# Performance work log

Hardware: AMD Instinct MI355X
Metric: run time of the kernel (lower is better)

## Reference

```python
import jax, jax.numpy as jnp
import numpy as np

D_MODEL = 16
D_STATE = 16
D_CONV = 4
EXPAND = 2
D_INNER = EXPAND * D_MODEL  # 32
DT_RANK = 1                 # ceil(d_model / 16)
H_MLP = 2 * D_MODEL         # MLP hidden = input_dim * 2
EPS = 1e-6
B, L = 16, 8192


def setup_inputs() -> dict:
    key = jax.random.key(0)
    ks = jax.random.split(key, 20)
    g = lambda i, shape, s: jax.random.normal(ks[i], shape, jnp.float32) * s
    # S4D-real init for A_log, as in mamba_ssm
    A_log = jnp.log(jnp.broadcast_to(jnp.arange(1, D_STATE + 1, dtype=jnp.float32), (D_INNER, D_STATE)))
    return {
        "x": jax.random.normal(ks[0], (B, L, D_MODEL), jnp.float32),
        "rms1_w": jnp.ones((D_MODEL,), jnp.float32),
        "in_proj_w": g(1, (D_MODEL, 2 * D_INNER), 0.25),
        "conv_w": g(2, (D_INNER, D_CONV), 0.3),
        "conv_b": g(3, (D_INNER,), 0.05),
        "x_proj_w": g(4, (D_INNER, DT_RANK + 2 * D_STATE), 0.2),
        "dt_proj_w": g(5, (DT_RANK, D_INNER), 0.5),
        "dt_proj_b": g(6, (D_INNER,), 0.1),
        "A_log": A_log,
        "D_skip": jnp.ones((D_INNER,), jnp.float32),
        "out_proj_w": g(7, (D_INNER, D_MODEL), 0.2),
        "rms2_w": jnp.ones((D_MODEL,), jnp.float32),
        "fc1_w": g(8, (D_MODEL, H_MLP), 0.25),
        "fc1_b": g(9, (H_MLP,), 0.05),
        "fc2_w": g(10, (H_MLP, H_MLP), 0.2),
        "fc2_b": g(11, (H_MLP,), 0.05),
        "fc3_w": g(12, (H_MLP, D_MODEL), 0.2),
        "fc3_b": g(13, (D_MODEL,), 0.05),
    }


def _rmsnorm(h, w):
    v = jnp.mean(h.astype(jnp.float32) ** 2, axis=-1, keepdims=True)
    return w * (h * jax.lax.rsqrt(v + EPS))


def _mamba(x0, in_proj_w, conv_w, conv_b, x_proj_w, dt_proj_w, dt_proj_b, A_log, D_skip, out_proj_w):
    b, l, _ = x0.shape
    xz = x0 @ in_proj_w                      # [B,L,2*Di]
    xm, z = jnp.split(xz, 2, axis=-1)        # each [B,L,Di]
    # causal depthwise conv1d (kernel D_CONV), padding d_conv-1, truncated to L
    xp = jnp.pad(xm, ((0, 0), (D_CONV - 1, 0), (0, 0)))
    xc = conv_b + sum(conv_w[:, k] * xp[:, k:k + l, :] for k in range(D_CONV))
    xc = jax.nn.silu(xc)
    # input-dependent dt, B, C
    proj = xc @ x_proj_w                     # [B,L,dt_rank+2*Ds]
    dt, Bm, Cm = jnp.split(proj, [DT_RANK, DT_RANK + D_STATE], axis=-1)
    dt = jax.nn.softplus(dt @ dt_proj_w + dt_proj_b)   # [B,L,Di]
    A = -jnp.exp(A_log)                      # [Di,Ds]
    deltaA = jnp.exp(dt[..., None] * A)                             # [B,L,Di,Ds]
    deltaBx = dt[..., None] * Bm[:, :, None, :] * xc[..., None]     # [B,L,Di,Ds]
    # sequential selective scan over time (time-major for lax.scan)
    def step(h, inputs):
        dA, dBx, C = inputs                  # [B,Di,Ds],[B,Di,Ds],[B,Ds]
        h = dA * h + dBx
        y = jnp.einsum('bds,bs->bd', h, C)
        return h, y
    h0 = jnp.zeros((b, D_INNER, D_STATE), xc.dtype)
    xs = (deltaA.transpose(1, 0, 2, 3), deltaBx.transpose(1, 0, 2, 3), Cm.transpose(1, 0, 2))
    _, ys = jax.lax.scan(step, h0, xs)       # [L,B,Di]
    y = ys.transpose(1, 0, 2) + D_skip * xc  # [B,L,Di]
    y = y * jax.nn.silu(z)
    return y @ out_proj_w                    # [B,L,Dm]


def reference(x, rms1_w, in_proj_w, conv_w, conv_b, x_proj_w, dt_proj_w, dt_proj_b,
              A_log, D_skip, out_proj_w, rms2_w, fc1_w, fc1_b, fc2_w, fc2_b, fc3_w, fc3_b):
    x0 = _rmsnorm(x, rms1_w)
    x1 = _mamba(x0, in_proj_w, conv_w, conv_b, x_proj_w, dt_proj_w, dt_proj_b, A_log, D_skip, out_proj_w)
    x = x1 + x
    x2 = _rmsnorm(x, rms2_w)
    h = jax.nn.relu(x2 @ fc1_w + fc1_b)
    h = jax.nn.relu(h @ fc2_w + fc2_b)
    x3 = h @ fc3_w + fc3_b
    return x + x3
```

## Files before the change

### kernel.cpp

```cpp
#include <hip/hip_runtime.h>

#define LSEQ 8192
#define NBAT 16
#define DMOD 16
#define DINN 32
#define DSTA 16
#define CL   32
#define NCH  (LSEQ / CL)
#define NCHT (NBAT * NCH)
#define NROWS (NBAT * LSEQ)
#define SUMN ((size_t)NCHT * 512)
#define NSEG 8
#define SEGC (NCH / NSEG)
#define RECU 800
#define LOG2E 1.44269504f

typedef __attribute__((ext_vector_type(8))) short bf16x8;
typedef __attribute__((ext_vector_type(4))) float f32x4;

__device__ __forceinline__ float fsilu(float v) { return v / (1.f + __expf(-v)); }
__device__ __forceinline__ float fsoftplus(float v) {
  return v > 20.f ? v : __logf(1.f + __expf(v));
}
__device__ __forceinline__ unsigned packbf(float a, float b) {
  unsigned r;
  asm("v_cvt_pk_bf16_f32 %0, %1, %2" : "=v"(r) : "v"(a), "v"(b));
  return r;
}
__device__ __forceinline__ short f2bf(float f) {
  return (short)(packbf(f, f) & 0xffffu);
}
__device__ __forceinline__ float bf2f(short s) {
  union { unsigned u; float f; } v;
  v.u = ((unsigned)(unsigned short)s) << 16;
  return v.f;
}
__device__ __forceinline__ float bflo(unsigned u) {
  union { unsigned a; float f; } v; v.a = u << 16; return v.f;
}
__device__ __forceinline__ float bfhi(unsigned u) {
  union { unsigned a; float f; } v; v.a = u & 0xffff0000u; return v.f;
}

__device__ __forceinline__ void load_x_row(const float* __restrict__ x, long r,
                                           float* __restrict__ xr) {
  const float4* xp = reinterpret_cast<const float4*>(x + r * DMOD);
  float4 v0 = xp[0], v1 = xp[1], v2 = xp[2], v3 = xp[3];
  xr[0] = v0.x; xr[1] = v0.y; xr[2] = v0.z; xr[3] = v0.w;
  xr[4] = v1.x; xr[5] = v1.y; xr[6] = v1.z; xr[7] = v1.w;
  xr[8] = v2.x; xr[9] = v2.y; xr[10] = v2.z; xr[11] = v2.w;
  xr[12] = v3.x; xr[13] = v3.y; xr[14] = v3.z; xr[15] = v3.w;
}

__device__ __forceinline__ f32x4 mm(bf16x8 a, bf16x8 b, f32x4 c) {
  return __builtin_amdgcn_mfma_f32_16x16x32_bf16(a, b, c, 0, 0, 0);
}
__device__ __forceinline__ bf16x8 bfrag(const float* __restrict__ W, int ldw,
                                        int coloff, int col, int kg, int kreal) {
  bf16x8 b = {0, 0, 0, 0, 0, 0, 0, 0};
#pragma unroll
  for (int e = 0; e < 8; e++) {
    int k = kg * 8 + e;
    if (k < kreal) b[e] = f2bf(W[k * ldw + coloff + col]);
  }
  return b;
}

__global__ __launch_bounds__(256) void k_prep(
    const float* __restrict__ x, const float* __restrict__ rms1w,
    const float* __restrict__ ipw, const float* __restrict__ cw,
    const float* __restrict__ cb, const float* __restrict__ xpw,
    const float* __restrict__ dtw, const float* __restrict__ dtb,
    const float* __restrict__ A_log, const float* __restrict__ Dskip,
    unsigned* __restrict__ rec, float* __restrict__ Pb,
    float* __restrict__ Hb) {
  __shared__ short xmv[67][36];
  __shared__ short x0b[64][40];
  __shared__ short xcb[64][40];
  int t = threadIdx.x;
  int lane = t & 63, wid = t >> 6;
  int col = lane & 15, kg = lane >> 4;
  long row0 = (long)blockIdx.x * 64;
  int l0 = (int)(row0 & (LSEQ - 1));
  const f32x4 zero4 = {0.f, 0.f, 0.f, 0.f};

  bf16x8 Bip0 = bfrag(ipw, 64, 0, col, kg, 16);
  bf16x8 Bip1 = bfrag(ipw, 64, 16, col, kg, 16);
  bf16x8 Bdt, Bb, Bc;
#pragma unroll
  for (int e = 0; e < 8; e++) {
    int k = kg * 8 + e;
    Bdt[e] = (col == 0) ? f2bf(xpw[k * 33]) : (short)0;
    Bb[e] = f2bf(xpw[k * 33 + 1 + col]);
    Bc[e] = f2bf(xpw[k * 33 + 17 + col]);
  }

  if (t < 128) {
    int row = t >> 1, hf = t & 1;
    const float4* xp =
        reinterpret_cast<const float4*>(x + (row0 + row) * DMOD + hf * 8);
    float4 v0 = xp[0], v1 = xp[1];
    float xr[8] = {v0.x, v0.y, v0.z, v0.w, v1.x, v1.y, v1.z, v1.w};
    float ss = 0.f;
#pragma unroll
    for (int i = 0; i < 8; i++) ss += xr[i] * xr[i];
    ss += __shfl_xor(ss, 1);
    float inv1 = rsqrtf(ss * (1.f / 16.f) + 1e-6f);
    unsigned u[4];
#pragma unroll
    for (int i = 0; i < 4; i++)
      u[i] = packbf(xr[2 * i] * inv1 * rms1w[hf * 8 + 2 * i],
                    xr[2 * i + 1] * inv1 * rms1w[hf * 8 + 2 * i + 1]);
    *reinterpret_cast<uint4*>(&x0b[row][hf * 8]) =
        make_uint4(u[0], u[1], u[2], u[3]);
  } else if (t < 224) {
    int h = (t - 128) >> 5, k = (t - 128) & 31;
    short v = 0;
    if (l0 != 0) {
      float xr[16];
      load_x_row(x, row0 - 3 + h, xr);
      float ss = 0.f;
#pragma unroll
      for (int i = 0; i < 16; i++) ss += xr[i] * xr[i];
      float inv1 = rsqrtf(ss * (1.f / 16.f) + 1e-6f);
      float acc = 0.f;
#pragma unroll
      for (int i = 0; i < 16; i++)
        acc = fmaf(xr[i] * inv1 * rms1w[i], ipw[i * 64 + k], acc);
      v = f2bf(acc);
    }
    xmv[h][k] = v;
  }
  __syncthreads();

  {
    int arow = wid * 16 + col;
    bf16x8 a = {0, 0, 0, 0, 0, 0, 0, 0};
    if (kg < 2) a = *reinterpret_cast<const bf16x8*>(&x0b[arow][kg * 8]);
    f32x4 m0 = mm(a, Bip0, zero4);
    f32x4 m1 = mm(a, Bip1, zero4);
    int orow = 3 + wid * 16 + kg * 4;
#pragma unroll
    for (int reg = 0; reg < 4; reg++) {
      unsigned p = packbf(m0[reg], m1[reg]);
      xmv[orow + reg][col] = (short)(p & 0xffffu);
      xmv[orow + reg][col + 16] = (short)(p >> 16);
    }
  }
  __syncthreads();

  {
    int row = t >> 2, q = t & 3;
    unsigned u[4];
#pragma unroll
    for (int dp = 0; dp < 4; dp++) {
      int d = q * 8 + dp * 2;
      float ce = cb[d], co = cb[d + 1];
#pragma unroll
      for (int k = 0; k < 4; k++) {
        unsigned xu = *reinterpret_cast<const unsigned*>(&xmv[row + k][d]);
        ce = fmaf(cw[d * 4 + k], bflo(xu), ce);
        co = fmaf(cw[(d + 1) * 4 + k], bfhi(xu), co);
      }
      u[dp] = packbf(fsilu(ce), fsilu(co));
    }
    *reinterpret_cast<uint4*>(&xcb[row][q * 8]) =
        make_uint4(u[0], u[1], u[2], u[3]);
  }
  __syncthreads();

  {
    int arow = wid * 16 + col;
    bf16x8 a2 = *reinterpret_cast<const bf16x8*>(&xcb[arow][kg * 8]);
    f32x4 pd = mm(a2, Bdt, zero4);
    f32x4 pb = mm(a2, Bb, zero4);
    f32x4 pc = mm(a2, Bc, zero4);
    int orow = wid * 16 + kg * 4;
#pragma unroll
    for (int reg = 0; reg < 4; reg++) {
      unsigned p = packbf(pb[reg], pc[reg]);
      xmv[orow + reg][col] = (short)(p & 0xffffu);
      xmv[orow + reg][16 + col] = (short)(p >> 16);
      if (col == 0) xmv[orow + reg][32] = f2bf(pd[reg]);
    }
  }
  __syncthreads();

  {
    int row = t >> 2, q = t & 3;
    float p0 = bf2f(xmv[row][32]);
    unsigned u[4];
#pragma unroll
    for (int dp = 0; dp < 4; dp++) {
      int d = q * 8 + dp * 2;
      u[dp] = packbf(fsoftplus(fmaf(p0, dtw[d], dtb[d])),
                     fsoftplus(fmaf(p0, dtw[d + 1], dtb[d + 1])));
    }
    *reinterpret_cast<uint4*>(&x0b[row][q * 8]) =
        make_uint4(u[0], u[1], u[2], u[3]);
  }
  __syncthreads();

  {
    int ch = t >> 7, b128 = t & 127;
    int d = b128 >> 2, s4 = (b128 & 3) << 2;
    float Ad0 = -__expf(A_log[d * 16 + s4 + 0]) * LOG2E;
    float Ad1 = -__expf(A_log[d * 16 + s4 + 1]) * LOG2E;
    float Ad2 = -__expf(A_log[d * 16 + s4 + 2]) * LOG2E;
    float Ad3 = -__expf(A_log[d * 16 + s4 + 3]) * LOG2E;
    float dskd = Dskip[d];
    bool w0 = (t & 3) == 0;
    float H0 = 0.f, H1 = 0.f, H2 = 0.f, H3 = 0.f, cum = 0.f;
#pragma unroll 4
    for (int li = 0; li < CL; li++) {
      int row = ch * CL + li;
      float dt = bf2f(x0b[row][d]);
      float xcv = bf2f(xcb[row][d]);
      float dx = dt * xcv;
      cum += dt;
      uint2 bu = *reinterpret_cast<const uint2*>(&xmv[row][s4]);
      uint2 cu = *reinterpret_cast<const uint2*>(&xmv[row][16 + s4]);
      float a;
      a = __builtin_amdgcn_exp2f(dt * Ad0); H0 = fmaf(a, H0, dx * bflo(bu.x));
      a = __builtin_amdgcn_exp2f(dt * Ad1); H1 = fmaf(a, H1, dx * bfhi(bu.x));
      a = __builtin_amdgcn_exp2f(dt * Ad2); H2 = fmaf(a, H2, dx * bflo(bu.y));
      a = __builtin_amdgcn_exp2f(dt * Ad3); H3 = fmaf(a, H3, dx * bfhi(bu.y));
      float py = bflo(cu.x) * H0;
      py = fmaf(bfhi(cu.x), H1, py);
      py = fmaf(bflo(cu.y), H2, py);
      py = fmaf(bfhi(cu.y), H3, py);
      py += __shfl_xor(py, 1);
      py += __shfl_xor(py, 2);
      if (w0) xcb[row][d] = f2bf(fmaf(dskd, xcv, py));
    }
    size_t sb_ = (size_t)(blockIdx.x * 2 + ch) * 512 + (size_t)(d * 16 + s4);
    *reinterpret_cast<float4*>(Pb + sb_) = make_float4(
        __builtin_amdgcn_exp2f(cum * Ad0), __builtin_amdgcn_exp2f(cum * Ad1),
        __builtin_amdgcn_exp2f(cum * Ad2), __builtin_amdgcn_exp2f(cum * Ad3));
    *reinterpret_cast<float4*>(Hb + sb_) = make_float4(H0, H1, H2, H3);
  }
  __syncthreads();

  {
    unsigned* rb0 = rec + (size_t)(blockIdx.x * 2) * RECU;
#pragma unroll
    for (int i = 0; i < 7; i++) {
      int idx = i * 256 + t;
      if (idx < 1600) {
        int ch = idx / 800;
        int rem = idx - ch * 800;
        int c = rem >> 5, l = rem & 31;
        int row = ch * 32 + l;
        unsigned val;
        if (c < 16)
          val = *reinterpret_cast<const unsigned*>(&xcb[row][2 * c]);
        else if (c < 24)
          val = *reinterpret_cast<const unsigned*>(&xmv[row][16 + 2 * (c - 16)]);
        else
          val = (unsigned)(unsigned short)xmv[row][32];
        rb0[ch * RECU + rem] = val;
      }
    }
  }
}

__global__ __launch_bounds__(256) void k_seg(float* __restrict__ Pb,
                                             float* __restrict__ Hb,
                                             float* __restrict__ segP,
                                             float* __restrict__ segH) {
  int g = blockIdx.x * 256 + threadIdx.x;
  int b = g >> 12;
  int rem = g & 4095;
  int seg = rem >> 9, st = rem & 511;
  size_t o = ((size_t)(b * NCH + seg * SEGC)) * 512 + st;
  float h = 0.f, p = 1.f;
#pragma unroll 4
  for (int c = 0; c < SEGC; c++) {
    float P = Pb[o], H = Hb[o];
    Pb[o] = p;
    Hb[o] = h;
    h = fmaf(P, h, H);
    p *= P;
    o += 512;
  }
  size_t so = (size_t)(b * NSEG + seg) * 512 + st;
  segP[so] = p;
  segH[so] = h;
}

__global__ __launch_bounds__(256) void k_carry(const float* __restrict__ segP,
                                               const float* __restrict__ segH,
                                               float* __restrict__ carry) {
  int g = blockIdx.x * 256 + threadIdx.x;
  int b = g >> 9, st = g & 511;
  float h = 0.f;
#pragma unroll
  for (int s = 0; s < NSEG; s++) {
    size_t so = (size_t)(b * NSEG + s) * 512 + st;
    carry[so] = h;
    h = fmaf(segP[so], h, segH[so]);
  }
}

__global__ __launch_bounds__(256) void k_mlp(
    const unsigned* __restrict__ rec, const float* __restrict__ x,
    const float* __restrict__ A_log, const float* __restrict__ Pb,
    const float* __restrict__ Hb, const float* __restrict__ carry,
    const float* __restrict__ dtw, const float* __restrict__ dtb,
    const float* __restrict__ rms1w, const float* __restrict__ ipw,
    const float* __restrict__ opw, const float* __restrict__ rms2w,
    const float* __restrict__ f1w, const float* __restrict__ f1b,
    const float* __restrict__ f2w, const float* __restrict__ f2b,
    const float* __restrict__ f3w, const float* __restrict__ f3b,
    float* __restrict__ out) {
  __shared__ float h0L[4 * 516];
  __shared__ float Ads[512];
  __shared__ short sbx[128][24];
  __shared__ short sby[128][40];
  int t = threadIdx.x, bc = blockIdx.x;
  long row0 = (long)bc * 128;

  Ads[t] = -__expf(A_log[t]) * LOG2E;
  Ads[256 + t] = -__expf(A_log[256 + t]) * LOG2E;
#pragma unroll
  for (int i = 0; i < 8; i++) {
    int idx = i * 256 + t;
    int chl = idx >> 9, st = idx & 511;
    int gc = bc * 4 + chl;
    size_t o = (size_t)gc * 512 + st;
    int b = gc >> 8, seg = (gc >> 5) & 7;
    h0L[chl * 516 + st] =
        fmaf(Pb[o], carry[(size_t)(b * NSEG + seg) * 512 + st], Hb[o]);
  }
  {
    int row = t >> 1, hf = t & 1;
    const float4* xp =
        reinterpret_cast<const float4*>(x + (row0 + row) * DMOD + hf * 8);
    float4 v0 = xp[0], v1 = xp[1];
    float xr[8] = {v0.x, v0.y, v0.z, v0.w, v1.x, v1.y, v1.z, v1.w};
    float ss = 0.f;
#pragma unroll
    for (int i = 0; i < 8; i++) ss += xr[i] * xr[i];
    ss += __shfl_xor(ss, 1);
    float inv1 = rsqrtf(ss * (1.f / 16.f) + 1e-6f);
    unsigned u[4];
#pragma unroll
    for (int i = 0; i < 4; i++)
      u[i] = packbf(xr[2 * i] * inv1 * rms1w[hf * 8 + 2 * i],
                    xr[2 * i + 1] * inv1 * rms1w[hf * 8 + 2 * i + 1]);
    *reinterpret_cast<uint4*>(&sbx[t >> 1][hf * 8]) =
        make_uint4(u[0], u[1], u[2], u[3]);
  }
  __syncthreads();

  {
    int ch = t >> 6, half = (t >> 5) & 1, l = t & 31;
    const unsigned* rb = rec + (size_t)(bc * 4 + ch) * RECU;
    float Cv[16];
#pragma unroll
    for (int c = 0; c < 8; c++) {
      unsigned u = rb[(16 + c) * 32 + l];
      Cv[2 * c] = bflo(u);
      Cv[2 * c + 1] = bfhi(u);
    }
    float p0 = bflo(rb[24 * 32 + l]);
    const float* h0c = &h0L[ch * 516];
    int row = ch * 32 + l;
#pragma unroll
    for (int cc = 0; cc < 8; cc++) {
      int c = half * 8 + cc;
      int d0 = 2 * c, d1 = 2 * c + 1;
      float cd0 = fsoftplus(fmaf(p0, dtw[d0], dtb[d0]));
      float cd1 = fsoftplus(fmaf(p0, dtw[d1], dtb[d1]));
#pragma unroll
      for (int dl = 1; dl < 32; dl <<= 1) {
        float u0 = __shfl_up(cd0, dl, 32);
        float u1 = __shfl_up(cd1, dl, 32);
        if (l >= dl) { cd0 += u0; cd1 += u1; }
      }
      unsigned yu = rb[c * 32 + l];
      float acc0 = bflo(yu), acc1 = bfhi(yu);
      int dof0 = d0 * 16, dof1 = d1 * 16;
#pragma unroll
      for (int s = 0; s < 16; s++) {
        float e0 = __builtin_amdgcn_exp2f(Ads[dof0 + s] * cd0);
        float e1 = __builtin_amdgcn_exp2f(Ads[dof1 + s] * cd1);
        acc0 = fmaf(e0 * Cv[s], h0c[dof0 + s], acc0);
        acc1 = fmaf(e1 * Cv[s], h0c[dof1 + s], acc1);
      }
      *reinterpret_cast<unsigned*>(&sby[row][2 * c]) = packbf(acc0, acc1);
    }
  }
  __syncthreads();

  {
    int lane = t & 63, w = t >> 6;
    int col = lane & 15, kg = lane >> 4;
    bf16x8 Bz0 = bfrag(ipw + 32, 64, 0, col, kg, 16);
    bf16x8 Bz1 = bfrag(ipw + 32, 64, 16, col, kg, 16);
    bf16x8 Bop = bfrag(opw, 16, 0, col, kg, 32);
    bf16x8 Bf1_0 = bfrag(f1w, 32, 0, col, kg, 16);
    bf16x8 Bf1_1 = bfrag(f1w, 32, 16, col, kg, 16);
    bf16x8 Bf2_0 = bfrag(f2w, 32, 0, col, kg, 32);
    bf16x8 Bf2_1 = bfrag(f2w, 32, 16, col, kg, 32);
    bf16x8 Bf3 = bfrag(f3w, 16, 0, col, kg, 32);
    float b1_0 = f1b[col], b1_1 = f1b[16 + col];
    float b2_0 = f2b[col], b2_1 = f2b[16 + col];
    float b3c = f3b[col], rw2 = rms2w[col];
    const f32x4 zero4 = {0.f, 0.f, 0.f, 0.f};
#pragma unroll 1
    for (int rt = 0; rt < 2; rt++) {
      int tile0 = w * 32 + rt * 16;
      bf16x8 ax0 = {0, 0, 0, 0, 0, 0, 0, 0};
      if (kg < 2) ax0 = *reinterpret_cast<const bf16x8*>(&sbx[tile0 + col][kg * 8]);
      f32x4 zf0 = mm(ax0, Bz0, zero4);
      f32x4 zf1 = mm(ax0, Bz1, zero4);
#pragma unroll
      for (int reg = 0; reg < 4; reg++) {
        int lrow = tile0 + kg * 4 + reg;
        float y0 = bf2f(sby[lrow][col]);
        float y1 = bf2f(sby[lrow][16 + col]);
        unsigned p = packbf(y0 * fsilu(zf0[reg]), y1 * fsilu(zf1[reg]));
        sby[lrow][col] = (short)(p & 0xffffu);
        sby[lrow][16 + col] = (short)(p >> 16);
      }
      bf16x8 ayo = *reinterpret_cast<const bf16x8*>(&sby[tile0 + col][kg * 8]);
      f32x4 x1f = mm(ayo, Bop, zero4);
      float xres[4];
#pragma unroll
      for (int reg = 0; reg < 4; reg++) {
        long grow = row0 + tile0 + kg * 4 + reg;
        xres[reg] = x1f[reg] + x[grow * 16 + col];
      }
#pragma unroll
      for (int reg = 0; reg < 4; reg++) {
        float ss = xres[reg] * xres[reg];
        ss += __shfl_xor(ss, 1);
        ss += __shfl_xor(ss, 2);
        ss += __shfl_xor(ss, 4);
        ss += __shfl_xor(ss, 8);
        float inv2 = rsqrtf(ss * (1.f / 16.f) + 1e-6f);
        sby[tile0 + kg * 4 + reg][col] = f2bf(xres[reg] * inv2 * rw2);
      }
      bf16x8 ax2 = {0, 0, 0, 0, 0, 0, 0, 0};
      if (kg < 2) ax2 = *reinterpret_cast<const bf16x8*>(&sby[tile0 + col][kg * 8]);
      f32x4 h1f0 = mm(ax2, Bf1_0, zero4);
      f32x4 h1f1 = mm(ax2, Bf1_1, zero4);
#pragma unroll
      for (int reg = 0; reg < 4; reg++) {
        int lrow = tile0 + kg * 4 + reg;
        unsigned p = packbf(fmaxf(h1f0[reg] + b1_0, 0.f),
                            fmaxf(h1f1[reg] + b1_1, 0.f));
        sby[lrow][col] = (short)(p & 0xffffu);
        sby[lrow][16 + col] = (short)(p >> 16);
      }
      bf16x8 ah1 = *reinterpret_cast<const bf16x8*>(&sby[tile0 + col][kg * 8]);
      f32x4 h2f0 = mm(ah1, Bf2_0, zero4);
      f32x4 h2f1 = mm(ah1, Bf2_1, zero4);
#pragma unroll
      for (int reg = 0; reg < 4; reg++) {
        int lrow = tile0 + kg * 4 + reg;
        unsigned p = packbf(fmaxf(h2f0[reg] + b2_0, 0.f),
                            fmaxf(h2f1[reg] + b2_1, 0.f));
        sby[lrow][col] = (short)(p & 0xffffu);
        sby[lrow][16 + col] = (short)(p >> 16);
      }
      bf16x8 ah2 = *reinterpret_cast<const bf16x8*>(&sby[tile0 + col][kg * 8]);
      f32x4 x3f = mm(ah2, Bf3, zero4);
#pragma unroll
      for (int reg = 0; reg < 4; reg++) {
        long grow = row0 + tile0 + kg * 4 + reg;
        out[grow * 16 + col] = xres[reg] + x3f[reg] + b3c;
      }
    }
  }
}

extern "C" void kernel_launch(void* const* d_in, const int* in_sizes, int n_in,
                              void* d_out, int out_size, void* d_ws,
                              size_t ws_size, hipStream_t stream) {
  const float* x = (const float*)d_in[0];
  const float* rms1w = (const float*)d_in[1];
  const float* ipw = (const float*)d_in[2];
  const float* cw = (const float*)d_in[3];
  const float* cb = (const float*)d_in[4];
  const float* xpw = (const float*)d_in[5];
  const float* dtw = (const float*)d_in[6];
  const float* dtb = (const float*)d_in[7];
  const float* A_log = (const float*)d_in[8];
  const float* Dskip = (const float*)d_in[9];
  const float* opw = (const float*)d_in[10];
  const float* rms2w = (const float*)d_in[11];
  const float* f1w = (const float*)d_in[12];
  const float* f1b = (const float*)d_in[13];
  const float* f2w = (const float*)d_in[14];
  const float* f2b = (const float*)d_in[15];
  const float* f3w = (const float*)d_in[16];
  const float* f3b = (const float*)d_in[17];
  float* out = (float*)d_out;

  unsigned* rec = (unsigned*)d_ws;
  float* Pb = (float*)(rec + (size_t)NCHT * RECU);
  float* Hb = Pb + SUMN;
  float* segP = Hb + SUMN;
  float* segH = segP + NBAT * NSEG * 512;
  float* carry = segH + NBAT * NSEG * 512;

  hipLaunchKernelGGL(k_prep, dim3(NROWS / 64), dim3(256), 0, stream, x, rms1w,
                     ipw, cw, cb, xpw, dtw, dtb, A_log, Dskip, rec, Pb, Hb);
  hipLaunchKernelGGL(k_seg, dim3(256), dim3(256), 0, stream, Pb, Hb, segP,
                     segH);
  hipLaunchKernelGGL(k_carry, dim3(32), dim3(256), 0, stream, segP, segH,
                     carry);
  hipLaunchKernelGGL(k_mlp, dim3(NROWS / 128), dim3(256), 0, stream, rec, x,
                     A_log, Pb, Hb, carry, dtw, dtb, rms1w, ipw, opw, rms2w,
                     f1w, f1b, f2w, f2b, f3w, f3b, out);
}
```

Measured before the change: 84.67 us.

## Use one 128-thread block per 32-row chunk in prep and MLP kernels

```diff
diff --git a/kernel.cpp b/kernel.cpp
--- a/kernel.cpp
+++ b/kernel.cpp
@@ -14,6 +14,7 @@
 #define SEGC (NCH / NSEG)
 #define RECU 800
 #define LOG2E 1.44269504f
+#define FENCE() asm volatile("" ::: "memory")
 
 typedef __attribute__((ext_vector_type(8))) short bf16x8;
 typedef __attribute__((ext_vector_type(4))) float f32x4;
@@ -66,7 +67,7 @@
   return b;
 }
 
-__global__ __launch_bounds__(256) void k_prep(
+__global__ __launch_bounds__(128) void k_prep(
     const float* __restrict__ x, const float* __restrict__ rms1w,
     const float* __restrict__ ipw, const float* __restrict__ cw,
     const float* __restrict__ cb, const float* __restrict__ xpw,
@@ -74,14 +75,15 @@
     const float* __restrict__ A_log, const float* __restrict__ Dskip,
     unsigned* __restrict__ rec, float* __restrict__ Pb,
     float* __restrict__ Hb) {
-  __shared__ short xmv[67][36];
-  __shared__ short x0b[64][40];
-  __shared__ short xcb[64][40];
+  __shared__ short XM[35][36];
+  __shared__ short X0[32][32];
+  __shared__ short XC[32][40];
   int t = threadIdx.x;
-  int lane = t & 63, wid = t >> 6;
-  int col = lane & 15, kg = lane >> 4;
-  long row0 = (long)blockIdx.x * 64;
-  int l0 = (int)(row0 & (LSEQ - 1));
+  int l = t & 63, wid = t >> 6;
+  int col = l & 15, kg = l >> 4;
+  int chunk = blockIdx.x;
+  long row0 = (long)chunk * CL;
+  bool first = (chunk & (NCH - 1)) == 0;
   const f32x4 zero4 = {0.f, 0.f, 0.f, 0.f};
 
   bf16x8 Bip0 = bfrag(ipw, 64, 0, col, kg, 16);
@@ -95,56 +97,49 @@
     Bc[e] = f2bf(xpw[k * 33 + 17 + col]);
   }
 
-  if (t < 128) {
-    int row = t >> 1, hf = t & 1;
+  {
+    int row = t >> 2, q = t & 3;
     const float4* xp =
-        reinterpret_cast<const float4*>(x + (row0 + row) * DMOD + hf * 8);
-    float4 v0 = xp[0], v1 = xp[1];
-    float xr[8] = {v0.x, v0.y, v0.z, v0.w, v1.x, v1.y, v1.z, v1.w};
-    float ss = 0.f;
-#pragma unroll
-    for (int i = 0; i < 8; i++) ss += xr[i] * xr[i];
+        reinterpret_cast<const float4*>(x + (row0 + row) * DMOD + q * 4);
+    float4 v = xp[0];
+    float ss = v.x * v.x + v.y * v.y + v.z * v.z + v.w * v.w;
     ss += __shfl_xor(ss, 1);
+    ss += __shfl_xor(ss, 2);
     float inv1 = rsqrtf(ss * (1.f / 16.f) + 1e-6f);
-    unsigned u[4];
-#pragma unroll
-    for (int i = 0; i < 4; i++)
-      u[i] = packbf(xr[2 * i] * inv1 * rms1w[hf * 8 + 2 * i],
-                    xr[2 * i + 1] * inv1 * rms1w[hf * 8 + 2 * i + 1]);
-    *reinterpret_cast<uint4*>(&x0b[row][hf * 8]) =
-        make_uint4(u[0], u[1], u[2], u[3]);
-  } else if (t < 224) {
-    int h = (t - 128) >> 5, k = (t - 128) & 31;
-    short v = 0;
-    if (l0 != 0) {
+    unsigned u0 = packbf(v.x * inv1 * rms1w[q * 4], v.y * inv1 * rms1w[q * 4 + 1]);
+    unsigned u1 = packbf(v.z * inv1 * rms1w[q * 4 + 2], v.w * inv1 * rms1w[q * 4 + 3]);
+    *reinterpret_cast<uint2*>(&X0[row][q * 4]) = make_uint2(u0, u1);
+  }
+  if (t < 96) {
+    int h = t >> 5, k = t & 31;
+    float a0 = 0.f;
+    if (!first) {
       float xr[16];
       load_x_row(x, row0 - 3 + h, xr);
       float ss = 0.f;
 #pragma unroll
       for (int i = 0; i < 16; i++) ss += xr[i] * xr[i];
       float inv1 = rsqrtf(ss * (1.f / 16.f) + 1e-6f);
-      float acc = 0.f;
 #pragma unroll
       for (int i = 0; i < 16; i++)
-        acc = fmaf(xr[i] * inv1 * rms1w[i], ipw[i * 64 + k], acc);
-      v = f2bf(acc);
-    }
-    xmv[h][k] = v;
-  }
-  __syncthreads();
+        a0 = fmaf(xr[i] * inv1 * rms1w[i], ipw[i * 64 + k], a0);
+    }
+    XM[h][k] = f2bf(a0);
+  }
+  FENCE();
 
   {
     int arow = wid * 16 + col;
     bf16x8 a = {0, 0, 0, 0, 0, 0, 0, 0};
-    if (kg < 2) a = *reinterpret_cast<const bf16x8*>(&x0b[arow][kg * 8]);
+    if (kg < 2) a = *reinterpret_cast<const bf16x8*>(&X0[arow][kg * 8]);
     f32x4 m0 = mm(a, Bip0, zero4);
     f32x4 m1 = mm(a, Bip1, zero4);
     int orow = 3 + wid * 16 + kg * 4;
 #pragma unroll
     for (int reg = 0; reg < 4; reg++) {
       unsigned p = packbf(m0[reg], m1[reg]);
-      xmv[orow + reg][col] = (short)(p & 0xffffu);
-      xmv[orow + reg][col + 16] = (short)(p >> 16);
+      XM[orow + reg][col] = (short)(p & 0xffffu);
+      XM[orow + reg][col + 16] = (short)(p >> 16);
     }
   }
   __syncthreads();
@@ -158,37 +153,36 @@
       float ce = cb[d], co = cb[d + 1];
 #pragma unroll
       for (int k = 0; k < 4; k++) {
-        unsigned xu = *reinterpret_cast<const unsigned*>(&xmv[row + k][d]);
+        unsigned xu = *reinterpret_cast<const unsigned*>(&XM[row + k][d]);
         ce = fmaf(cw[d * 4 + k], bflo(xu), ce);
         co = fmaf(cw[(d + 1) * 4 + k], bfhi(xu), co);
       }
       u[dp] = packbf(fsilu(ce), fsilu(co));
     }
-    *reinterpret_cast<uint4*>(&xcb[row][q * 8]) =
-        make_uint4(u[0], u[1], u[2], u[3]);
+    *reinterpret_cast<uint4*>(&XC[row][q * 8]) = make_uint4(u[0], u[1], u[2], u[3]);
   }
   __syncthreads();
 
   {
     int arow = wid * 16 + col;
-    bf16x8 a2 = *reinterpret_cast<const bf16x8*>(&xcb[arow][kg * 8]);
+    bf16x8 a2 = *reinterpret_cast<const bf16x8*>(&XC[arow][kg * 8]);
     f32x4 pd = mm(a2, Bdt, zero4);
     f32x4 pb = mm(a2, Bb, zero4);
     f32x4 pc = mm(a2, Bc, zero4);
-    int orow = wid * 16 + kg * 4;
+    int orow = 3 + wid * 16 + kg * 4;
 #pragma unroll
     for (int reg = 0; reg < 4; reg++) {
       unsigned p = packbf(pb[reg], pc[reg]);
-      xmv[orow + reg][col] = (short)(p & 0xffffu);
-      xmv[orow + reg][16 + col] = (short)(p >> 16);
-      if (col == 0) xmv[orow + reg][32] = f2bf(pd[reg]);
-    }
-  }
-  __syncthreads();
+      XM[orow + reg][col] = (short)(p & 0xffffu);
+      XM[orow + reg][16 + col] = (short)(p >> 16);
+      if (col == 0) XM[orow + reg][32] = f2bf(pd[reg]);
+    }
+  }
+  FENCE();
 
   {
     int row = t >> 2, q = t & 3;
-    float p0 = bf2f(xmv[row][32]);
+    float p0 = bf2f(XM[3 + row][32]);
     unsigned u[4];
 #pragma unroll
     for (int dp = 0; dp < 4; dp++) {
@@ -196,44 +190,40 @@
       u[dp] = packbf(fsoftplus(fmaf(p0, dtw[d], dtb[d])),
                      fsoftplus(fmaf(p0, dtw[d + 1], dtb[d + 1])));
     }
-    *reinterpret_cast<uint4*>(&x0b[row][q * 8]) =
-        make_uint4(u[0], u[1], u[2], u[3]);
+    *reinterpret_cast<uint4*>(&X0[row][q * 8]) = make_uint4(u[0], u[1], u[2], u[3]);
   }
   __syncthreads();
 
   {
-    int ch = t >> 7, b128 = t & 127;
-    int d = b128 >> 2, s4 = (b128 & 3) << 2;
-    float Ad0 = -__expf(A_log[d * 16 + s4 + 0]) * LOG2E;
-    float Ad1 = -__expf(A_log[d * 16 + s4 + 1]) * LOG2E;
-    float Ad2 = -__expf(A_log[d * 16 + s4 + 2]) * LOG2E;
-    float Ad3 = -__expf(A_log[d * 16 + s4 + 3]) * LOG2E;
+    int d = t >> 2, s4 = (t & 3) << 2;
+    float4 al = *reinterpret_cast<const float4*>(A_log + d * DSTA + s4);
+    float Ad0 = -__expf(al.x) * LOG2E, Ad1 = -__expf(al.y) * LOG2E;
+    float Ad2 = -__expf(al.z) * LOG2E, Ad3 = -__expf(al.w) * LOG2E;
     float dskd = Dskip[d];
-    bool w0 = (t & 3) == 0;
+    bool wy = (t & 3) == 0;
     float H0 = 0.f, H1 = 0.f, H2 = 0.f, H3 = 0.f, cum = 0.f;
 #pragma unroll 4
     for (int li = 0; li < CL; li++) {
-      int row = ch * CL + li;
-      float dt = bf2f(x0b[row][d]);
-      float xcv = bf2f(xcb[row][d]);
+      float dt = bf2f(X0[li][d]);
+      float xcv = bf2f(XC[li][d]);
       float dx = dt * xcv;
       cum += dt;
-      uint2 bu = *reinterpret_cast<const uint2*>(&xmv[row][s4]);
-      uint2 cu = *reinterpret_cast<const uint2*>(&xmv[row][16 + s4]);
+      uint2 bu = *reinterpret_cast<const uint2*>(&XM[3 + li][s4]);
+      uint2 cu = *reinterpret_cast<const uint2*>(&XM[3 + li][16 + s4]);
       float a;
       a = __builtin_amdgcn_exp2f(dt * Ad0); H0 = fmaf(a, H0, dx * bflo(bu.x));
       a = __builtin_amdgcn_exp2f(dt * Ad1); H1 = fmaf(a, H1, dx * bfhi(bu.x));
       a = __builtin_amdgcn_exp2f(dt * Ad2); H2 = fmaf(a, H2, dx * bflo(bu.y));
       a = __builtin_amdgcn_exp2f(dt * Ad3); H3 = fmaf(a, H3, dx * bfhi(bu.y));
-      float py = bflo(cu.x) * H0;
-      py = fmaf(bfhi(cu.x), H1, py);
-      py = fmaf(bflo(cu.y), H2, py);
-      py = fmaf(bfhi(cu.y), H3, py);
-      py += __shfl_xor(py, 1);
-      py += __shfl_xor(py, 2);
-      if (w0) xcb[row][d] = f2bf(fmaf(dskd, xcv, py));
-    }
-    size_t sb_ = (size_t)(blockIdx.x * 2 + ch) * 512 + (size_t)(d * 16 + s4);
+      float y = bflo(cu.x) * H0;
+      y = fmaf(bfhi(cu.x), H1, y);
+      y = fmaf(bflo(cu.y), H2, y);
+      y = fmaf(bfhi(cu.y), H3, y);
+      y += __shfl_xor(y, 1);
+      y += __shfl_xor(y, 2);
+      if (wy) XC[li][d] = f2bf(fmaf(dskd, xcv, y));
+    }
+    size_t sb_ = (size_t)chunk * 512 + (size_t)(d * 16 + s4);
     *reinterpret_cast<float4*>(Pb + sb_) = make_float4(
         __builtin_amdgcn_exp2f(cum * Ad0), __builtin_amdgcn_exp2f(cum * Ad1),
         __builtin_amdgcn_exp2f(cum * Ad2), __builtin_amdgcn_exp2f(cum * Ad3));
@@ -242,23 +232,20 @@
   __syncthreads();
 
   {
-    unsigned* rb0 = rec + (size_t)(blockIdx.x * 2) * RECU;
+    unsigned* rb = rec + (size_t)chunk * RECU;
 #pragma unroll
     for (int i = 0; i < 7; i++) {
-      int idx = i * 256 + t;
-      if (idx < 1600) {
-        int ch = idx / 800;
-        int rem = idx - ch * 800;
-        int c = rem >> 5, l = rem & 31;
-        int row = ch * 32 + l;
+      int idx = i * 128 + t;
+      if (idx < 800) {
+        int c = idx >> 5, r = idx & 31;
         unsigned val;
         if (c < 16)
-          val = *reinterpret_cast<const unsigned*>(&xcb[row][2 * c]);
+          val = *reinterpret_cast<const unsigned*>(&XC[r][2 * c]);
         else if (c < 24)
-          val = *reinterpret_cast<const unsigned*>(&xmv[row][16 + 2 * (c - 16)]);
+          val = *reinterpret_cast<const unsigned*>(&XM[3 + r][16 + 2 * (c - 16)]);
         else
-          val = (unsigned)(unsigned short)xmv[row][32];
-        rb0[ch * RECU + rem] = val;
+          val = (unsigned)(unsigned short)XM[3 + r][32];
+        rb[idx] = val;
       }
     }
   }
@@ -302,7 +289,7 @@
   }
 }
 
-__global__ __launch_bounds__(256) void k_mlp(
+__global__ __launch_bounds__(128) void k_mlp(
     const unsigned* __restrict__ rec, const float* __restrict__ x,
     const float* __restrict__ A_log, const float* __restrict__ Pb,
     const float* __restrict__ Hb, const float* __restrict__ carry,
@@ -313,62 +300,60 @@
     const float* __restrict__ f2w, const float* __restrict__ f2b,
     const float* __restrict__ f3w, const float* __restrict__ f3b,
     float* __restrict__ out) {
-  __shared__ float h0L[4 * 516];
   __shared__ float Ads[512];
-  __shared__ short sbx[128][24];
-  __shared__ short sby[128][40];
-  int t = threadIdx.x, bc = blockIdx.x;
-  long row0 = (long)bc * 128;
-
-  Ads[t] = -__expf(A_log[t]) * LOG2E;
-  Ads[256 + t] = -__expf(A_log[256 + t]) * LOG2E;
-#pragma unroll
-  for (int i = 0; i < 8; i++) {
-    int idx = i * 256 + t;
-    int chl = idx >> 9, st = idx & 511;
-    int gc = bc * 4 + chl;
-    size_t o = (size_t)gc * 512 + st;
+  __shared__ float h0w[512];
+  __shared__ short sbx[32][24];
+  __shared__ short sby[32][40];
+  int t = threadIdx.x;
+  int l = t & 63, wid = t >> 6;
+  int gc = blockIdx.x;
+  long row0 = (long)gc * CL;
+
+#pragma unroll
+  for (int i = 0; i < 4; i++) {
+    int idx = i * 128 + t;
+    Ads[idx] = -__expf(A_log[idx]) * LOG2E;
+  }
+  {
+    size_t o = (size_t)gc * 512 + (size_t)(t * 4);
     int b = gc >> 8, seg = (gc >> 5) & 7;
-    h0L[chl * 516 + st] =
-        fmaf(Pb[o], carry[(size_t)(b * NSEG + seg) * 512 + st], Hb[o]);
-  }
-  {
-    int row = t >> 1, hf = t & 1;
+    size_t co = (size_t)(b * NSEG + seg) * 512 + (size_t)(t * 4);
+    float4 pv = *reinterpret_cast<const float4*>(Pb + o);
+    float4 hv = *reinterpret_cast<const float4*>(Hb + o);
+    float4 cv = *reinterpret_cast<const float4*>(carry + co);
+    *reinterpret_cast<float4*>(&h0w[t * 4]) =
+        make_float4(fmaf(pv.x, cv.x, hv.x), fmaf(pv.y, cv.y, hv.y),
+                    fmaf(pv.z, cv.z, hv.z), fmaf(pv.w, cv.w, hv.w));
+  }
+  {
+    int row = t >> 2, q = t & 3;
     const float4* xp =
-        reinterpret_cast<const float4*>(x + (row0 + row) * DMOD + hf * 8);
-    float4 v0 = xp[0], v1 = xp[1];
-    float xr[8] = {v0.x, v0.y, v0.z, v0.w, v1.x, v1.y, v1.z, v1.w};
-    float ss = 0.f;
-#pragma unroll
-    for (int i = 0; i < 8; i++) ss += xr[i] * xr[i];
+        reinterpret_cast<const float4*>(x + (row0 + row) * DMOD + q * 4);
+    float4 v = xp[0];
+    float ss = v.x * v.x + v.y * v.y + v.z * v.z + v.w * v.w;
     ss += __shfl_xor(ss, 1);
+    ss += __shfl_xor(ss, 2);
     float inv1 = rsqrtf(ss * (1.f / 16.f) + 1e-6f);
-    unsigned u[4];
-#pragma unroll
-    for (int i = 0; i < 4; i++)
-      u[i] = packbf(xr[2 * i] * inv1 * rms1w[hf * 8 + 2 * i],
-                    xr[2 * i + 1] * inv1 * rms1w[hf * 8 + 2 * i + 1]);
-    *reinterpret_cast<uint4*>(&sbx[t >> 1][hf * 8]) =
-        make_uint4(u[0], u[1], u[2], u[3]);
+    unsigned u0 = packbf(v.x * inv1 * rms1w[q * 4], v.y * inv1 * rms1w[q * 4 + 1]);
+    unsigned u1 = packbf(v.z * inv1 * rms1w[q * 4 + 2], v.w * inv1 * rms1w[q * 4 + 3]);
+    *reinterpret_cast<uint2*>(&sbx[row][q * 4]) = make_uint2(u0, u1);
   }
   __syncthreads();
 
   {
-    int ch = t >> 6, half = (t >> 5) & 1, l = t & 31;
-    const unsigned* rb = rec + (size_t)(bc * 4 + ch) * RECU;
+    int half = t >> 5, r = t & 31;
+    const unsigned* rb = rec + (size_t)gc * RECU;
     float Cv[16];
 #pragma unroll
     for (int c = 0; c < 8; c++) {
-      unsigned u = rb[(16 + c) * 32 + l];
+      unsigned u = rb[(16 + c) * 32 + r];
       Cv[2 * c] = bflo(u);
       Cv[2 * c + 1] = bfhi(u);
     }
-    float p0 = bflo(rb[24 * 32 + l]);
-    const float* h0c = &h0L[ch * 516];
-    int row = ch * 32 + l;
-#pragma unroll
-    for (int cc = 0; cc < 8; cc++) {
-      int c = half * 8 + cc;
+    float p0 = bflo(rb[24 * 32 + r]);
+#pragma unroll
+    for (int cc = 0; cc < 4; cc++) {
+      int c = half * 4 + cc;
       int d0 = 2 * c, d1 = 2 * c + 1;
       float cd0 = fsoftplus(fmaf(p0, dtw[d0], dtb[d0]));
       float cd1 = fsoftplus(fmaf(p0, dtw[d1], dtb[d1]));
@@ -376,26 +361,25 @@
       for (int dl = 1; dl < 32; dl <<= 1) {
         float u0 = __shfl_up(cd0, dl, 32);
         float u1 = __shfl_up(cd1, dl, 32);
-        if (l >= dl) { cd0 += u0; cd1 += u1; }
+        if (r >= dl) { cd0 += u0; cd1 += u1; }
       }
-      unsigned yu = rb[c * 32 + l];
+      unsigned yu = rb[c * 32 + r];
       float acc0 = bflo(yu), acc1 = bfhi(yu);
       int dof0 = d0 * 16, dof1 = d1 * 16;
 #pragma unroll
       for (int s = 0; s < 16; s++) {
         float e0 = __builtin_amdgcn_exp2f(Ads[dof0 + s] * cd0);
         float e1 = __builtin_amdgcn_exp2f(Ads[dof1 + s] * cd1);
-        acc0 = fmaf(e0 * Cv[s], h0c[dof0 + s], acc0);
-        acc1 = fmaf(e1 * Cv[s], h0c[dof1 + s], acc1);
+        acc0 = fmaf(e0 * Cv[s], h0w[dof0 + s], acc0);
+        acc1 = fmaf(e1 * Cv[s], h0w[dof1 + s], acc1);
       }
-      *reinterpret_cast<unsigned*>(&sby[row][2 * c]) = packbf(acc0, acc1);
+      *reinterpret_cast<unsigned*>(&sby[r][2 * c]) = packbf(acc0, acc1);
     }
   }
   __syncthreads();
 
   {
-    int lane = t & 63, w = t >> 6;
-    int col = lane & 15, kg = lane >> 4;
+    int col = l & 15, kg = l >> 4;
     bf16x8 Bz0 = bfrag(ipw + 32, 64, 0, col, kg, 16);
     bf16x8 Bz1 = bfrag(ipw + 32, 64, 16, col, kg, 16);
     bf16x8 Bop = bfrag(opw, 16, 0, col, kg, 32);
@@ -408,70 +392,73 @@
     float b2_0 = f2b[col], b2_1 = f2b[16 + col];
     float b3c = f3b[col], rw2 = rms2w[col];
     const f32x4 zero4 = {0.f, 0.f, 0.f, 0.f};
-#pragma unroll 1
-    for (int rt = 0; rt < 2; rt++) {
-      int tile0 = w * 32 + rt * 16;
-      bf16x8 ax0 = {0, 0, 0, 0, 0, 0, 0, 0};
-      if (kg < 2) ax0 = *reinterpret_cast<const bf16x8*>(&sbx[tile0 + col][kg * 8]);
-      f32x4 zf0 = mm(ax0, Bz0, zero4);
-      f32x4 zf1 = mm(ax0, Bz1, zero4);
-#pragma unroll
-      for (int reg = 0; reg < 4; reg++) {
-        int lrow = tile0 + kg * 4 + reg;
-        float y0 = bf2f(sby[lrow][col]);
-        float y1 = bf2f(sby[lrow][16 + col]);
-        unsigned p = packbf(y0 * fsilu(zf0[reg]), y1 * fsilu(zf1[reg]));
-        sby[lrow][col] = (short)(p & 0xffffu);
-        sby[lrow][16 + col] = (short)(p >> 16);
-      }
-      bf16x8 ayo = *reinterpret_cast<const bf16x8*>(&sby[tile0 + col][kg * 8]);
-      f32x4 x1f = mm(ayo, Bop, zero4);
-      float xres[4];
-#pragma unroll
-      for (int reg = 0; reg < 4; reg++) {
-        long grow = row0 + tile0 + kg * 4 + reg;
-        xres[reg] = x1f[reg] + x[grow * 16 + col];
-      }
-#pragma unroll
-      for (int reg = 0; reg < 4; reg++) {
-        float ss = xres[reg] * xres[reg];
-        ss += __shfl_xor(ss, 1);
-        ss += __shfl_xor(ss, 2);
-        ss += __shfl_xor(ss, 4);
-        ss += __shfl_xor(ss, 8);
-        float inv2 = rsqrtf(ss * (1.f / 16.f) + 1e-6f);
-        sby[tile0 + kg * 4 + reg][col] = f2bf(xres[reg] * inv2 * rw2);
-      }
-      bf16x8 ax2 = {0, 0, 0, 0, 0, 0, 0, 0};
-      if (kg < 2) ax2 = *reinterpret_cast<const bf16x8*>(&sby[tile0 + col][kg * 8]);
-      f32x4 h1f0 = mm(ax2, Bf1_0, zero4);
-      f32x4 h1f1 = mm(ax2, Bf1_1, zero4);
-#pragma unroll
-      for (int reg = 0; reg < 4; reg++) {
-        int lrow = tile0 + kg * 4 + reg;
-        unsigned p = packbf(fmaxf(h1f0[reg] + b1_0, 0.f),
-                            fmaxf(h1f1[reg] + b1_1, 0.f));
-        sby[lrow][col] = (short)(p & 0xffffu);
-        sby[lrow][16 + col] = (short)(p >> 16);
-      }
-      bf16x8 ah1 = *reinterpret_cast<const bf16x8*>(&sby[tile0 + col][kg * 8]);
-      f32x4 h2f0 = mm(ah1, Bf2_0, zero4);
-      f32x4 h2f1 = mm(ah1, Bf2_1, zero4);
-#pragma unroll
-      for (int reg = 0; reg < 4; reg++) {
-        int lrow = tile0 + kg * 4 + reg;
-        unsigned p = packbf(fmaxf(h2f0[reg] + b2_0, 0.f),
-                            fmaxf(h2f1[reg] + b2_1, 0.f));
-        sby[lrow][col] = (short)(p & 0xffffu);
-        sby[lrow][16 + col] = (short)(p >> 16);
-      }
-      bf16x8 ah2 = *reinterpret_cast<const bf16x8*>(&sby[tile0 + col][kg * 8]);
-      f32x4 x3f = mm(ah2, Bf3, zero4);
-#pragma unroll
-      for (int reg = 0; reg < 4; reg++) {
-        long grow = row0 + tile0 + kg * 4 + reg;
-        out[grow * 16 + col] = xres[reg] + x3f[reg] + b3c;
-      }
+    int tile0 = wid * 16;
+    bf16x8 ax0 = {0, 0, 0, 0, 0, 0, 0, 0};
+    if (kg < 2)
+      ax0 = *reinterpret_cast<const bf16x8*>(&sbx[tile0 + col][kg * 8]);
+    f32x4 zf0 = mm(ax0, Bz0, zero4);
+    f32x4 zf1 = mm(ax0, Bz1, zero4);
+#pragma unroll
+    for (int reg = 0; reg < 4; reg++) {
+      int lrow = tile0 + kg * 4 + reg;
+      float y0 = bf2f(sby[lrow][col]);
+      float y1 = bf2f(sby[lrow][16 + col]);
+      unsigned p = packbf(y0 * fsilu(zf0[reg]), y1 * fsilu(zf1[reg]));
+      sby[lrow][col] = (short)(p & 0xffffu);
+      sby[lrow][16 + col] = (short)(p >> 16);
+    }
+    FENCE();
+    bf16x8 ayo = *reinterpret_cast<const bf16x8*>(&sby[tile0 + col][kg * 8]);
+    f32x4 x1f = mm(ayo, Bop, zero4);
+    float xres[4];
+#pragma unroll
+    for (int reg = 0; reg < 4; reg++) {
+      long grow = row0 + tile0 + kg * 4 + reg;
+      xres[reg] = x1f[reg] + x[grow * 16 + col];
+    }
+#pragma unroll
+    for (int reg = 0; reg < 4; reg++) {
+      float ss = xres[reg] * xres[reg];
+      ss += __shfl_xor(ss, 1);
+      ss += __shfl_xor(ss, 2);
+      ss += __shfl_xor(ss, 4);
+      ss += __shfl_xor(ss, 8);
+      float inv2 = rsqrtf(ss * (1.f / 16.f) + 1e-6f);
+      sby[tile0 + kg * 4 + reg][col] = f2bf(xres[reg] * inv2 * rw2);
+    }
+    FENCE();
+    bf16x8 ax2 = {0, 0, 0, 0, 0, 0, 0, 0};
+    if (kg < 2)
+      ax2 = *reinterpret_cast<const bf16x8*>(&sby[tile0 + col][kg * 8]);
+    f32x4 h1f0 = mm(ax2, Bf1_0, zero4);
+    f32x4 h1f1 = mm(ax2, Bf1_1, zero4);
+#pragma unroll
+    for (int reg = 0; reg < 4; reg++) {
+      int lrow = tile0 + kg * 4 + reg;
+      unsigned p = packbf(fmaxf(h1f0[reg] + b1_0, 0.f),
+                          fmaxf(h1f1[reg] + b1_1, 0.f));
+      sby[lrow][col] = (short)(p & 0xffffu);
+      sby[lrow][16 + col] = (short)(p >> 16);
+    }
+    FENCE();
+    bf16x8 ah1 = *reinterpret_cast<const bf16x8*>(&sby[tile0 + col][kg * 8]);
+    f32x4 h2f0 = mm(ah1, Bf2_0, zero4);
+    f32x4 h2f1 = mm(ah1, Bf2_1, zero4);
+#pragma unroll
+    for (int reg = 0; reg < 4; reg++) {
+      int lrow = tile0 + kg * 4 + reg;
+      unsigned p = packbf(fmaxf(h2f0[reg] + b2_0, 0.f),
+                          fmaxf(h2f1[reg] + b2_1, 0.f));
+      sby[lrow][col] = (short)(p & 0xffffu);
+      sby[lrow][16 + col] = (short)(p >> 16);
+    }
+    FENCE();
+    bf16x8 ah2 = *reinterpret_cast<const bf16x8*>(&sby[tile0 + col][kg * 8]);
+    f32x4 x3f = mm(ah2, Bf3, zero4);
+#pragma unroll
+    for (int reg = 0; reg < 4; reg++) {
+      long grow = row0 + tile0 + kg * 4 + reg;
+      out[grow * 16 + col] = xres[reg] + x3f[reg] + b3c;
     }
   }
 }
@@ -506,13 +493,13 @@
   float* segH = segP + NBAT * NSEG * 512;
   float* carry = segH + NBAT * NSEG * 512;
 
-  hipLaunchKernelGGL(k_prep, dim3(NROWS / 64), dim3(256), 0, stream, x, rms1w,
-                     ipw, cw, cb, xpw, dtw, dtb, A_log, Dskip, rec, Pb, Hb);
+  hipLaunchKernelGGL(k_prep, dim3(NCHT), dim3(128), 0, stream, x, rms1w, ipw,
+                     cw, cb, xpw, dtw, dtb, A_log, Dskip, rec, Pb, Hb);
   hipLaunchKernelGGL(k_seg, dim3(256), dim3(256), 0, stream, Pb, Hb, segP,
                      segH);
   hipLaunchKernelGGL(k_carry, dim3(32), dim3(256), 0, stream, segP, segH,
                      carry);
-  hipLaunchKernelGGL(k_mlp, dim3(NROWS / 128), dim3(256), 0, stream, rec, x,
-                     A_log, Pb, Hb, carry, dtw, dtb, rms1w, ipw, opw, rms2w,
-                     f1w, f1b, f2w, f2b, f3w, f3b, out);
-}
+  hipLaunchKernelGGL(k_mlp, dim3(NCHT), dim3(128), 0, stream, rec, x, A_log,
+                     Pb, Hb, carry, dtw, dtb, rms1w, ipw, opw, rms2w, f1w, f1b,
+                     f2w, f2b, f3w, f3b, out);
+}
```

After: 91.56 us. 1.08x slower.
